# Kernel tuning notes

Hardware: AMD Instinct MI355X
Metric: run time of the kernel (lower is better)

## Reference

```python
import jax, jax.numpy as jnp
import numpy as np

H, C = 4, 32            # heads, per-head out channels
N, E = 25000, 400000    # nodes, edges
NODE_DIM, EDGE_DIM = 256, 64
HC = H * C
IN_DIMS = [NODE_DIM, NODE_DIM + HC, NODE_DIM + HC]


def _conv(h, src, dst, ea, Wq, bq, Wk, bk, Wv, bv, We, Ws, bs):
    """One PyG-style TransformerConv (concat=True, root_weight=True, beta=False)."""
    n = h.shape[0]
    q = (h @ Wq + bq).reshape(n, H, C)
    k = (h @ Wk + bk).reshape(n, H, C)
    v = (h @ Wv + bv).reshape(n, H, C)
    e = (ea @ We).reshape(-1, H, C)            # lin_edge has no bias in PyG
    kj = k[src] + e                             # (E,H,C) key + edge feature
    alpha = jnp.einsum('ehc,ehc->eh', q[dst], kj) / jnp.asarray(np.sqrt(C), h.dtype)
    # segment softmax over incoming edges of each destination node
    amax = jax.ops.segment_max(alpha, dst, num_segments=n)
    ex = jnp.exp(alpha - amax[dst])
    denom = jax.ops.segment_sum(ex, dst, num_segments=n)
    a = ex / (denom[dst] + 1e-16)
    msg = (v[src] + e) * a[:, :, None]          # (E,H,C)
    out = jax.ops.segment_sum(msg, dst, num_segments=n).reshape(n, HC)
    return out + h @ Ws + bs                    # root/skip connection


def setup_inputs() -> dict:
    key = jax.random.key(0)
    ks = iter(jax.random.split(key, 64))
    inp = {}
    inp['x'] = jax.random.normal(next(ks), (N, NODE_DIM), dtype=jnp.float32)
    inp['edge_index'] = jax.random.randint(next(ks), (2, E), 0, N, dtype=jnp.int64)
    inp['edge_attr'] = jax.random.normal(next(ks), (E, EDGE_DIM), dtype=jnp.float32)
    s = 0.05
    for i, din in enumerate(IN_DIMS):
        inp[f'Wq{i}'] = jax.random.normal(next(ks), (din, HC), dtype=jnp.float32) * s
        inp[f'bq{i}'] = jnp.zeros((HC,), jnp.float32)
        inp[f'Wk{i}'] = jax.random.normal(next(ks), (din, HC), dtype=jnp.float32) * s
        inp[f'bk{i}'] = jnp.zeros((HC,), jnp.float32)
        inp[f'Wv{i}'] = jax.random.normal(next(ks), (din, HC), dtype=jnp.float32) * s
        inp[f'bv{i}'] = jnp.zeros((HC,), jnp.float32)
        inp[f'We{i}'] = jax.random.normal(next(ks), (EDGE_DIM, HC), dtype=jnp.float32) * s
        inp[f'Ws{i}'] = jax.random.normal(next(ks), (din, HC), dtype=jnp.float32) * s
        inp[f'bs{i}'] = jnp.zeros((HC,), jnp.float32)
    inp['Wout'] = jax.random.normal(next(ks), (HC, C), dtype=jnp.float32) * s
    inp['bout'] = jnp.zeros((C,), jnp.float32)
    return inp


def reference(x, edge_index, edge_attr,
              Wq0, bq0, Wk0, bk0, Wv0, bv0, We0, Ws0, bs0,
              Wq1, bq1, Wk1, bk1, Wv1, bv1, We1, Ws1, bs1,
              Wq2, bq2, Wk2, bk2, Wv2, bv2, We2, Ws2, bs2,
              Wout, bout):
    src, dst = edge_index[0], edge_index[1]
    params = [
        (Wq0, bq0, Wk0, bk0, Wv0, bv0, We0, Ws0, bs0),
        (Wq1, bq1, Wk1, bk1, Wv1, bv1, We1, Ws1, bs1),
        (Wq2, bq2, Wk2, bk2, Wv2, bv2, We2, Ws2, bs2),
    ]
    h = _conv(x, src, dst, edge_attr, *params[0])
    for p in params[1:]:
        h = _conv(jnp.concatenate([h, x], axis=-1), src, dst, edge_attr, *p)
    return h @ Wout + bout  # (N, output_dim)
```

## Files before the change

kernel.cpp:

```cpp
#include <hip/hip_runtime.h>
#include <hip/hip_bf16.h>
#include <math.h>

#define HCX 128
#define EDX 64
#define KPAD 384

typedef short bf16x8 __attribute__((ext_vector_type(8)));
typedef float f32x4  __attribute__((ext_vector_type(4)));

__device__ __forceinline__ short f2bf(float v) {
    __hip_bfloat16 b = __float2bfloat16(v);
    return *reinterpret_cast<short*>(&b);
}
__device__ __forceinline__ float bf2f(short s) {
    __hip_bfloat16 b = *reinterpret_cast<__hip_bfloat16*>(&s);
    return __bfloat162float(b);
}
__device__ __forceinline__ void gload16(const short* g, short* l) {
    __builtin_amdgcn_global_load_lds((const __attribute__((address_space(1))) void*)g,
                                     (__attribute__((address_space(3))) void*)l, 16, 0, 0);
}
__device__ __forceinline__ float dot4(float4 a, float4 b) {
    return a.x * b.x + a.y * b.y + a.z * b.z + a.w * b.w;
}

__global__ __launch_bounds__(256) void k_zero_deg(int* __restrict__ deg, int n) {
    int t = blockIdx.x * 256 + threadIdx.x;
    if (t < n) deg[t] = 0;
}

__global__ __launch_bounds__(256) void k_hist(const int* __restrict__ dst, int* __restrict__ deg, int nE) {
    int t = blockIdx.x * 256 + threadIdx.x;
    if (t < nE) atomicAdd(&deg[dst[t]], 1);
}

__global__ __launch_bounds__(1024) void k_scan(const int* __restrict__ deg, int* __restrict__ csr_off,
                                               int* __restrict__ cursor, int nN) {
    __shared__ int sums[1024];
    int t = threadIdx.x;
    int chunk = (nN + 1023) >> 10;
    int lo = min(t * chunk, nN), hi = min(lo + chunk, nN);
    int s = 0;
    for (int i = lo; i < hi; ++i) s += deg[i];
    sums[t] = s;
    __syncthreads();
    for (int off = 1; off < 1024; off <<= 1) {
        int v = (t >= off) ? sums[t - off] : 0;
        __syncthreads();
        sums[t] += v;
        __syncthreads();
    }
    int run = (t == 0) ? 0 : sums[t - 1];
    for (int i = lo; i < hi; ++i) {
        csr_off[i] = run; cursor[i] = run;
        run += deg[i];
    }
    if (t == 1023) csr_off[nN] = sums[1023];
}

__global__ __launch_bounds__(256) void k_scatter(const int* __restrict__ dst, const int* __restrict__ src,
                                                 int* __restrict__ cursor,
                                                 int* __restrict__ edge_sorted, int* __restrict__ src_sorted,
                                                 int* __restrict__ dst_sorted, int nE) {
    int t = blockIdx.x * 256 + threadIdx.x;
    if (t < nE) {
        int d = dst[t];
        int pos = atomicAdd(&cursor[d], 1);
        edge_sorted[pos] = t;
        src_sorted[pos]  = src[t];
        dst_sorted[pos]  = d;
    }
}

__global__ __launch_bounds__(256) void k_gather_ea(const float* __restrict__ ea,
                                                   const int* __restrict__ edge_sorted,
                                                   float* __restrict__ ea_s, int nE)
{
    int t = blockIdx.x * 256 + threadIdx.x;
    int i = t >> 4, c = (t & 15) * 4;
    if (i < nE) {
        int eid = edge_sorted[i];
        *(float4*)(ea_s + (size_t)i * EDX + c) = *(const float4*)(ea + (size_t)eid * EDX + c);
    }
}

__global__ __launch_bounds__(256) void k_cvt_h(const float* __restrict__ pH, int has_h,
                                               short* __restrict__ Ah, short* __restrict__ Al,
                                               int nN, int Mpad)
{
    int t = blockIdx.x * 256 + threadIdx.x;
    int row = t >> 5;
    if (row >= Mpad) return;
    int c0 = (t & 31) * 4;
    float4 v = make_float4(0.f, 0.f, 0.f, 0.f);
    if (has_h && row < nN) v = *(const float4*)(pH + (size_t)row * HCX + c0);
    short4 hs, ls;
    hs.x = f2bf(v.x); ls.x = f2bf(v.x - bf2f(hs.x));
    hs.y = f2bf(v.y); ls.y = f2bf(v.y - bf2f(hs.y));
    hs.z = f2bf(v.z); ls.z = f2bf(v.z - bf2f(hs.z));
    hs.w = f2bf(v.w); ls.w = f2bf(v.w - bf2f(hs.w));
    *(short4*)(Ah + (size_t)row * KPAD + c0) = hs;
    *(short4*)(Al + (size_t)row * KPAD + c0) = ls;
}

__global__ __launch_bounds__(256) void k_cvt_x(const float* __restrict__ x,
                                               short* __restrict__ Ah, short* __restrict__ Al,
                                               int nN, int Mpad)
{
    int t = blockIdx.x * 256 + threadIdx.x;
    int row = t >> 6;
    if (row >= Mpad) return;
    int c0 = (t & 63) * 4;
    float4 v = make_float4(0.f, 0.f, 0.f, 0.f);
    if (row < nN) v = *(const float4*)(x + (size_t)row * 256 + c0);
    short4 hs, ls;
    hs.x = f2bf(v.x); ls.x = f2bf(v.x - bf2f(hs.x));
    hs.y = f2bf(v.y); ls.y = f2bf(v.y - bf2f(hs.y));
    hs.z = f2bf(v.z); ls.z = f2bf(v.z - bf2f(hs.z));
    hs.w = f2bf(v.w); ls.w = f2bf(v.w - bf2f(hs.w));
    *(short4*)(Ah + (size_t)row * KPAD + 128 + c0) = hs;
    *(short4*)(Al + (size_t)row * KPAD + 128 + c0) = ls;
}

__global__ __launch_bounds__(384) void k_cvt_W(const float* __restrict__ Wq, const float* __restrict__ Wk,
                                               const float* __restrict__ Wv, const float* __restrict__ Ws,
                                               int koff, int dinW,
                                               short* __restrict__ Wth, short* __restrict__ Wtl)
{
    int col = blockIdx.x;
    int g = col >> 7, c = col & 127;
    const float* W = (g == 0) ? Wq : (g == 1) ? Wk : (g == 2) ? Wv : Ws;
    for (int k = threadIdx.x; k < KPAD; k += blockDim.x) {
        int kr = k - koff;
        float v = (kr >= 0 && kr < dinW) ? W[(size_t)kr * HCX + c] : 0.f;
        short h = f2bf(v);
        Wth[(size_t)col * KPAD + k] = h;
        Wtl[(size_t)col * KPAD + k] = f2bf(v - bf2f(h));
    }
}

__global__ __launch_bounds__(256) void k_gemm(
    const short* __restrict__ Ah, const short* __restrict__ Al,
    const short* __restrict__ Wth, const short* __restrict__ Wtl,
    const float* __restrict__ bq, const float* __restrict__ bk,
    const float* __restrict__ bv, const float* __restrict__ bs,
    float* __restrict__ qkvs, int nN)
{
    __shared__ short AsH[128 * 32];
    __shared__ short AsL[128 * 32];
    __shared__ short BsH[128 * 32];
    __shared__ short BsL[128 * 32];

    const int rowB = blockIdx.x * 128;
    const int g = blockIdx.y;
    const int colB = g * 128;
    const int tid = threadIdx.x;
    const int w = tid >> 6, l = tid & 63;

    f32x4 acc[4][4];
    #pragma unroll
    for (int i = 0; i < 4; ++i)
        #pragma unroll
        for (int j = 0; j < 4; ++j)
            acc[i][j] = (f32x4){0.f, 0.f, 0.f, 0.f};

    const int lrow4 = l >> 2;
    const int gch = (l & 3) ^ ((l >> 3) & 3);
    const int lr = l & 15, kg = l >> 4;

    for (int ks = 0; ks < KPAD / 32; ++ks) {
        const int k0 = ks * 32;
        #pragma unroll
        for (int jj = 0; jj < 2; ++jj) {
            int j = w + jj * 4;
            int rr = j * 16 + lrow4;
            size_t aoff = (size_t)(rowB + rr) * KPAD + k0 + gch * 8;
            size_t boff = (size_t)(colB + rr) * KPAD + k0 + gch * 8;
            gload16(Ah  + aoff, AsH + j * 512);
            gload16(Al  + aoff, AsL + j * 512);
            gload16(Wth + boff, BsH + j * 512);
            gload16(Wtl + boff, BsL + j * 512);
        }
        __syncthreads();

        bf16x8 ah[4], am[4], bh[4], bm[4];
        #pragma unroll
        for (int mi = 0; mi < 4; ++mi) {
            int r = (w >> 1) * 64 + mi * 16 + lr;
            int ch = kg ^ ((r >> 1) & 3);
            int off = r * 32 + ch * 8;
            ah[mi] = *(const bf16x8*)(AsH + off);
            am[mi] = *(const bf16x8*)(AsL + off);
        }
        #pragma unroll
        for (int ni = 0; ni < 4; ++ni) {
            int c = (w & 1) * 64 + ni * 16 + lr;
            int ch = kg ^ ((c >> 1) & 3);
            int off = c * 32 + ch * 8;
            bh[ni] = *(const bf16x8*)(BsH + off);
            bm[ni] = *(const bf16x8*)(BsL + off);
        }
        #pragma unroll
        for (int mi = 0; mi < 4; ++mi)
            #pragma unroll
            for (int ni = 0; ni < 4; ++ni) {
                acc[mi][ni] = __builtin_amdgcn_mfma_f32_16x16x32_bf16(ah[mi], bh[ni], acc[mi][ni], 0, 0, 0);
                acc[mi][ni] = __builtin_amdgcn_mfma_f32_16x16x32_bf16(ah[mi], bm[ni], acc[mi][ni], 0, 0, 0);
                acc[mi][ni] = __builtin_amdgcn_mfma_f32_16x16x32_bf16(am[mi], bh[ni], acc[mi][ni], 0, 0, 0);
            }
        __syncthreads();
    }

    const float* bias = (g == 0) ? bq : (g == 1) ? bk : (g == 2) ? bv : bs;
    float* outp = qkvs + (size_t)g * nN * HCX;
    const int lq = l >> 4;
    #pragma unroll
    for (int mi = 0; mi < 4; ++mi)
        #pragma unroll
        for (int ni = 0; ni < 4; ++ni) {
            int c = (w & 1) * 64 + ni * 16 + lr;
            float bb = bias[c];
            #pragma unroll
            for (int j = 0; j < 4; ++j) {
                int r = rowB + (w >> 1) * 64 + mi * 16 + lq * 4 + j;
                if (r < nN) outp[(size_t)r * HCX + c] = acc[mi][ni][j] + bb;
            }
        }
}

__global__ __launch_bounds__(256) void k_qwe(const float* __restrict__ qpl,
                                             const float* __restrict__ We,
                                             float* __restrict__ qWe, int nN)
{
    __shared__ float Wes[64 * 128];
    __shared__ float qs[16][128];
    for (int i = threadIdx.x; i < 64 * 128; i += 256) {
        int d = i >> 7, c = i & 127;
        Wes[d * 128 + ((c + d) & 127)] = We[i];
    }
    int nb = blockIdx.x * 16;
    for (int i = threadIdx.x; i < 16 * 128; i += 256) {
        int r = i >> 7, c = i & 127;
        int row = nb + r;
        qs[r][c] = (row < nN) ? qpl[(size_t)row * HCX + c] : 0.f;
    }
    __syncthreads();
    int h = threadIdx.x >> 6, d = threadIdx.x & 63;
    const int base = h * 32;
    for (int r = 0; r < 16; ++r) {
        int row = nb + r;
        if (row >= nN) break;
        float s = 0.f;
        #pragma unroll
        for (int c = 0; c < 32; ++c)
            s += qs[r][base + c] * Wes[d * 128 + ((base + c + d) & 127)];
        qWe[(size_t)row * 256 + threadIdx.x] = s;
    }
}

__global__ __launch_bounds__(256) void k_alpha2(
    const float* __restrict__ qkvs, const float* __restrict__ qWe,
    const float* __restrict__ eaS,
    const int* __restrict__ eidx,
    const int* __restrict__ src_sorted, const int* __restrict__ dst_sorted,
    float* __restrict__ expA, int nN, int nE)
{
    int i = blockIdx.x * 256 + threadIdx.x;
    if (i >= nE) return;
    int sn = src_sorted[i], dn = dst_sorted[i];
    int erow = eidx ? eidx[i] : i;

    const float* q = qkvs + (size_t)dn * HCX;
    const float* k = qkvs + (size_t)nN * HCX + (size_t)sn * HCX;
    float r[4];
    #pragma unroll
    for (int h = 0; h < 4; ++h) {
        float4 s4 = make_float4(0.f, 0.f, 0.f, 0.f);
        #pragma unroll
        for (int c = 0; c < 32; c += 4) {
            float4 qv = *(const float4*)(q + h * 32 + c);
            float4 kv = *(const float4*)(k + h * 32 + c);
            s4.x += qv.x * kv.x; s4.y += qv.y * kv.y;
            s4.z += qv.z * kv.z; s4.w += qv.w * kv.w;
        }
        r[h] = s4.x + s4.y + s4.z + s4.w;
    }

    const float* qw = qWe + (size_t)dn * 256;
    const float* ev = eaS + (size_t)erow * EDX;
    float th0 = 0.f, th1 = 0.f, th2 = 0.f, th3 = 0.f;
    #pragma unroll
    for (int d0 = 0; d0 < 64; d0 += 16) {
        float4 a0 = *(const float4*)(ev + d0);
        float4 a1 = *(const float4*)(ev + d0 + 4);
        float4 a2 = *(const float4*)(ev + d0 + 8);
        float4 a3 = *(const float4*)(ev + d0 + 12);
        th0 += dot4(a0, *(const float4*)(qw +   0 + d0)) + dot4(a1, *(const float4*)(qw +   0 + d0 + 4))
             + dot4(a2, *(const float4*)(qw +   0 + d0 + 8)) + dot4(a3, *(const float4*)(qw +   0 + d0 + 12));
        th1 += dot4(a0, *(const float4*)(qw +  64 + d0)) + dot4(a1, *(const float4*)(qw +  64 + d0 + 4))
             + dot4(a2, *(const float4*)(qw +  64 + d0 + 8)) + dot4(a3, *(const float4*)(qw +  64 + d0 + 12));
        th2 += dot4(a0, *(const float4*)(qw + 128 + d0)) + dot4(a1, *(const float4*)(qw + 128 + d0 + 4))
             + dot4(a2, *(const float4*)(qw + 128 + d0 + 8)) + dot4(a3, *(const float4*)(qw + 128 + d0 + 12));
        th3 += dot4(a0, *(const float4*)(qw + 192 + d0)) + dot4(a1, *(const float4*)(qw + 192 + d0 + 4))
             + dot4(a2, *(const float4*)(qw + 192 + d0 + 8)) + dot4(a3, *(const float4*)(qw + 192 + d0 + 12));
    }

    const float scale = 0.17677669529663687f;
    float4 out;
    out.x = __expf((r[0] + th0) * scale);
    out.y = __expf((r[1] + th1) * scale);
    out.z = __expf((r[2] + th2) * scale);
    out.w = __expf((r[3] + th3) * scale);
    *(float4*)(expA + (size_t)i * 4) = out;
}

__global__ __launch_bounds__(256) void k_edge2(
    const float* __restrict__ qkvs, const float* __restrict__ expA,
    const float* __restrict__ eaS, const int* __restrict__ eidx,
    const float* __restrict__ We,
    const int* __restrict__ csr_off, const int* __restrict__ src_sorted,
    float* __restrict__ hout, int nN)
{
    __shared__ float wea_s[4][4][64];
    const int wv = threadIdx.x >> 6, l = threadIdx.x & 63;
    const int n = blockIdx.x * 4 + wv;
    const bool active = n < nN;
    int o0 = 0, o1 = 0;
    if (active) { o0 = csr_off[n]; o1 = csr_off[n + 1]; }

    const float* vpl = qkvs + 2 * (size_t)nN * HCX;
    const int hsel = l >> 5;

    float den0 = 0.f, den1 = 0.f, den2 = 0.f, den3 = 0.f;
    float w0 = 0.f, w1 = 0.f, w2 = 0.f, w3 = 0.f;
    float macc0 = 0.f, macc1 = 0.f;

    #pragma unroll 2
    for (int i = o0; i < o1; ++i) {
        float4 e4 = *(const float4*)(expA + (size_t)i * 4);
        int erow = eidx ? eidx[i] : i;
        int sn  = src_sorted[i];
        float eav = eaS[(size_t)erow * EDX + l];
        float vv0 = vpl[(size_t)sn * HCX + l];
        float vv1 = vpl[(size_t)sn * HCX + 64 + l];

        den0 += e4.x; den1 += e4.y; den2 += e4.z; den3 += e4.w;
        w0 += e4.x * eav; w1 += e4.y * eav; w2 += e4.z * eav; w3 += e4.w * eav;
        float eA = hsel ? e4.y : e4.x;
        float eB = hsel ? e4.w : e4.z;
        macc0 += eA * vv0;
        macc1 += eB * vv1;
    }

    wea_s[wv][0][l] = w0; wea_s[wv][1][l] = w1;
    wea_s[wv][2][l] = w2; wea_s[wv][3][l] = w3;
    __syncthreads();

    float acc1 = macc0, acc2 = macc1;
    const int h1 = hsel, h2 = 2 + hsel;
    #pragma unroll 8
    for (int d = 0; d < 64; ++d) {
        acc1 += wea_s[wv][h1][d] * We[d * HCX + l];
        acc2 += wea_s[wv][h2][d] * We[d * HCX + 64 + l];
    }
    if (active) {
        float d1 = (hsel ? den1 : den0) + 1e-16f;
        float d2 = (hsel ? den3 : den2) + 1e-16f;
        const float* spl = qkvs + 3 * (size_t)nN * HCX + (size_t)n * HCX;
        hout[(size_t)n * HCX + l]      = acc1 / d1 + spl[l];
        hout[(size_t)n * HCX + 64 + l] = acc2 / d2 + spl[64 + l];
    }
}

__global__ __launch_bounds__(256) void k_out(const float* __restrict__ h,
                                             const float* __restrict__ Wout,
                                             const float* __restrict__ bout,
                                             float* __restrict__ out, int nN)
{
    __shared__ float hs[8][128];
    int nb = blockIdx.x * 8;
    for (int i = threadIdx.x; i < 8 * 128; i += 256) {
        int r = i >> 7, c = i & 127;
        int row = nb + r;
        hs[r][c] = (row < nN) ? h[(size_t)row * 128 + c] : 0.f;
    }
    __syncthreads();
    int r = threadIdx.x >> 5, col = threadIdx.x & 31;
    int row = nb + r;
    if (row < nN) {
        float s = bout[col];
        #pragma unroll 16
        for (int c = 0; c < 128; ++c) s += hs[r][c] * Wout[c * 32 + col];
        out[(size_t)row * 32 + col] = s;
    }
}

static inline size_t align_up(size_t v, size_t a) { return (v + a - 1) & ~(a - 1); }

extern "C" void kernel_launch(void* const* d_in, const int* in_sizes, int n_in,
                              void* d_out, int out_size, void* d_ws, size_t ws_size,
                              hipStream_t stream)
{
    const float* x  = (const float*)d_in[0];
    const int*   ei = (const int*)d_in[1];
    const float* ea = (const float*)d_in[2];
    const int nN = in_sizes[0] / 256;
    const int nE = in_sizes[1] / 2;
    const int Mpad = (nN + 127) & ~127;
    const int* src = ei;
    const int* dst = ei + nE;

    char* p = (char*)d_ws;
    size_t off = 0;
    auto take = [&](size_t bytes) { void* r = p + off; off = align_up(off + bytes, 256); return r; };
    int* csr_off     = (int*)take((size_t)(nN + 1) * 4);
    int* cursor      = (int*)take((size_t)nN * 4);
    int* deg         = (int*)take((size_t)nN * 4);
    int* edge_sorted = (int*)take((size_t)nE * 4);
    int* src_sorted  = (int*)take((size_t)nE * 4);
    int* dst_sorted  = (int*)take((size_t)nE * 4);
    float* qkvs = (float*)take((size_t)4 * nN * HCX * 4);
    float* qWe  = (float*)take((size_t)nN * 256 * 4);
    float* expA = (float*)take((size_t)nE * 4 * 4);
    float* h0   = (float*)take((size_t)nN * HCX * 4);
    float* h1   = (float*)take((size_t)nN * HCX * 4);
    short* Ah   = (short*)take((size_t)Mpad * KPAD * 2);
    short* Al   = (short*)take((size_t)Mpad * KPAD * 2);
    short* Wth  = (short*)take((size_t)512 * KPAD * 2);
    short* Wtl  = (short*)take((size_t)512 * KPAD * 2);
    float* ea_s = (float*)take((size_t)nE * EDX * 4);
    const bool use_sorted = (off <= ws_size);
    (void)n_in; (void)out_size;

    k_zero_deg<<<(nN + 255) / 256, 256, 0, stream>>>(deg, nN);
    k_hist<<<(nE + 255) / 256, 256, 0, stream>>>(dst, deg, nE);
    k_scan<<<1, 1024, 0, stream>>>(deg, csr_off, cursor, nN);
    k_scatter<<<(nE + 255) / 256, 256, 0, stream>>>(dst, src, cursor,
                                                    edge_sorted, src_sorted, dst_sorted, nE);

    const float* eaS = use_sorted ? ea_s : ea;
    const int* eidx  = use_sorted ? nullptr : edge_sorted;
    if (use_sorted)
        k_gather_ea<<<(nE * 16 + 255) / 256, 256, 0, stream>>>(ea, edge_sorted, ea_s, nE);

    k_cvt_x<<<(Mpad * 64 + 255) / 256, 256, 0, stream>>>(x, Ah, Al, nN, Mpad);

    auto layer = [&](const float* pH, int has_h, int base, float* hout) {
        const float* Wq = (const float*)d_in[base + 0];
        const float* bq = (const float*)d_in[base + 1];
        const float* Wk = (const float*)d_in[base + 2];
        const float* bk = (const float*)d_in[base + 3];
        const float* Wv = (const float*)d_in[base + 4];
        const float* bv = (const float*)d_in[base + 5];
        const float* We = (const float*)d_in[base + 6];
        const float* Ws = (const float*)d_in[base + 7];
        const float* bs = (const float*)d_in[base + 8];
        int koff = has_h ? 0 : 128;
        int dinW = has_h ? 384 : 256;
        k_cvt_h<<<(Mpad * 32 + 255) / 256, 256, 0, stream>>>(pH, has_h, Ah, Al, nN, Mpad);
        k_cvt_W<<<512, 384, 0, stream>>>(Wq, Wk, Wv, Ws, koff, dinW, Wth, Wtl);
        dim3 gg(Mpad / 128, 4);
        k_gemm<<<gg, 256, 0, stream>>>(Ah, Al, Wth, Wtl, bq, bk, bv, bs, qkvs, nN);
        k_qwe<<<(nN + 15) / 16, 256, 0, stream>>>(qkvs, We, qWe, nN);
        k_alpha2<<<(nE + 255) / 256, 256, 0, stream>>>(qkvs, qWe, eaS, eidx,
                                                       src_sorted, dst_sorted, expA, nN, nE);
        k_edge2<<<(nN + 3) / 4, 256, 0, stream>>>(qkvs, expA, eaS, eidx, We,
                                                  csr_off, src_sorted, hout, nN);
    };

    layer(nullptr, 0, 3,  h0);
    layer(h0, 1,   12, h1);
    layer(h1, 1,   21, h0);

    k_out<<<(nN + 7) / 8, 256, 0, stream>>>(h0, (const float*)d_in[30], (const float*)d_in[31],
                                            (float*)d_out, nN);
}
```

Before: 1.167 ms.

## Store sorted edge attributes as bf16 and split alpha kernel per head pair

The gathered, dst-sorted edge attribute copy is now stored as bf16 instead of fp32, halving the memory traffic of edge-attribute reads in both the alpha and aggregation kernels. The alpha kernel now uses two threads per edge, each handling two heads, which raises parallelism and cuts per-thread register pressure. bf16-to-float conversion is replaced with a plain shift. Precision of the edge attributes drops to bf16, which risks accuracy drift across three layers.

```diff
diff --git a/kernel.cpp b/kernel.cpp
--- a/kernel.cpp
+++ b/kernel.cpp
@@ -14,8 +14,8 @@
     return *reinterpret_cast<short*>(&b);
 }
 __device__ __forceinline__ float bf2f(short s) {
-    __hip_bfloat16 b = *reinterpret_cast<__hip_bfloat16*>(&s);
-    return __bfloat162float(b);
+    unsigned int u = ((unsigned int)(unsigned short)s) << 16;
+    return __uint_as_float(u);
 }
 __device__ __forceinline__ void gload16(const short* g, short* l) {
     __builtin_amdgcn_global_load_lds((const __attribute__((address_space(1))) void*)g,
@@ -73,15 +73,18 @@
     }
 }
 
-__global__ __launch_bounds__(256) void k_gather_ea(const float* __restrict__ ea,
-                                                   const int* __restrict__ edge_sorted,
-                                                   float* __restrict__ ea_s, int nE)
+__global__ __launch_bounds__(256) void k_gather_ea16(const float* __restrict__ ea,
+                                                     const int* __restrict__ edge_sorted,
+                                                     short* __restrict__ ea16, int nE)
 {
     int t = blockIdx.x * 256 + threadIdx.x;
     int i = t >> 4, c = (t & 15) * 4;
     if (i < nE) {
         int eid = edge_sorted[i];
-        *(float4*)(ea_s + (size_t)i * EDX + c) = *(const float4*)(ea + (size_t)eid * EDX + c);
+        float4 v = *(const float4*)(ea + (size_t)eid * EDX + c);
+        short4 s;
+        s.x = f2bf(v.x); s.y = f2bf(v.y); s.z = f2bf(v.z); s.w = f2bf(v.w);
+        *(short4*)(ea16 + (size_t)i * EDX + c) = s;
     }
 }
 
@@ -259,65 +262,67 @@
     }
 }
 
-__global__ __launch_bounds__(256) void k_alpha2(
+__global__ __launch_bounds__(256) void k_alpha3(
     const float* __restrict__ qkvs, const float* __restrict__ qWe,
-    const float* __restrict__ eaS,
+    const short* __restrict__ ea16,
+    const float* __restrict__ eaF,
     const int* __restrict__ eidx,
     const int* __restrict__ src_sorted, const int* __restrict__ dst_sorted,
     float* __restrict__ expA, int nN, int nE)
 {
-    int i = blockIdx.x * 256 + threadIdx.x;
+    int t = blockIdx.x * 256 + threadIdx.x;
+    int i = t >> 1, hp = t & 1;
     if (i >= nE) return;
     int sn = src_sorted[i], dn = dst_sorted[i];
-    int erow = eidx ? eidx[i] : i;
-
-    const float* q = qkvs + (size_t)dn * HCX;
-    const float* k = qkvs + (size_t)nN * HCX + (size_t)sn * HCX;
-    float r[4];
+
+    const float* q = qkvs + (size_t)dn * HCX + hp * 64;
+    const float* k = qkvs + (size_t)nN * HCX + (size_t)sn * HCX + hp * 64;
+    float r0 = 0.f, r1 = 0.f;
     #pragma unroll
-    for (int h = 0; h < 4; ++h) {
-        float4 s4 = make_float4(0.f, 0.f, 0.f, 0.f);
-        #pragma unroll
-        for (int c = 0; c < 32; c += 4) {
-            float4 qv = *(const float4*)(q + h * 32 + c);
-            float4 kv = *(const float4*)(k + h * 32 + c);
-            s4.x += qv.x * kv.x; s4.y += qv.y * kv.y;
-            s4.z += qv.z * kv.z; s4.w += qv.w * kv.w;
-        }
-        r[h] = s4.x + s4.y + s4.z + s4.w;
-    }
-
-    const float* qw = qWe + (size_t)dn * 256;
-    const float* ev = eaS + (size_t)erow * EDX;
-    float th0 = 0.f, th1 = 0.f, th2 = 0.f, th3 = 0.f;
-    #pragma unroll
-    for (int d0 = 0; d0 < 64; d0 += 16) {
-        float4 a0 = *(const float4*)(ev + d0);
-        float4 a1 = *(const float4*)(ev + d0 + 4);
-        float4 a2 = *(const float4*)(ev + d0 + 8);
-        float4 a3 = *(const float4*)(ev + d0 + 12);
-        th0 += dot4(a0, *(const float4*)(qw +   0 + d0)) + dot4(a1, *(const float4*)(qw +   0 + d0 + 4))
-             + dot4(a2, *(const float4*)(qw +   0 + d0 + 8)) + dot4(a3, *(const float4*)(qw +   0 + d0 + 12));
-        th1 += dot4(a0, *(const float4*)(qw +  64 + d0)) + dot4(a1, *(const float4*)(qw +  64 + d0 + 4))
-             + dot4(a2, *(const float4*)(qw +  64 + d0 + 8)) + dot4(a3, *(const float4*)(qw +  64 + d0 + 12));
-        th2 += dot4(a0, *(const float4*)(qw + 128 + d0)) + dot4(a1, *(const float4*)(qw + 128 + d0 + 4))
-             + dot4(a2, *(const float4*)(qw + 128 + d0 + 8)) + dot4(a3, *(const float4*)(qw + 128 + d0 + 12));
-        th3 += dot4(a0, *(const float4*)(qw + 192 + d0)) + dot4(a1, *(const float4*)(qw + 192 + d0 + 4))
-             + dot4(a2, *(const float4*)(qw + 192 + d0 + 8)) + dot4(a3, *(const float4*)(qw + 192 + d0 + 12));
+    for (int c = 0; c < 32; c += 4) {
+        r0 += dot4(*(const float4*)(q + c),      *(const float4*)(k + c));
+        r1 += dot4(*(const float4*)(q + 32 + c), *(const float4*)(k + 32 + c));
+    }
+
+    const float* qw = qWe + (size_t)dn * 256 + hp * 128;
+    float t0 = 0.f, t1 = 0.f;
+    if (ea16) {
+        const short* ev = ea16 + (size_t)i * EDX;
+        #pragma unroll
+        for (int d0 = 0; d0 < 64; d0 += 8) {
+            bf16x8 a8 = *(const bf16x8*)(ev + d0);
+            float4 qa = *(const float4*)(qw + d0);
+            float4 qb = *(const float4*)(qw + d0 + 4);
+            float4 qc = *(const float4*)(qw + 64 + d0);
+            float4 qd = *(const float4*)(qw + 64 + d0 + 4);
+            float a0 = bf2f(a8[0]), a1 = bf2f(a8[1]), a2 = bf2f(a8[2]), a3 = bf2f(a8[3]);
+            float a4 = bf2f(a8[4]), a5 = bf2f(a8[5]), a6 = bf2f(a8[6]), a7 = bf2f(a8[7]);
+            t0 += a0 * qa.x + a1 * qa.y + a2 * qa.z + a3 * qa.w
+                + a4 * qb.x + a5 * qb.y + a6 * qb.z + a7 * qb.w;
+            t1 += a0 * qc.x + a1 * qc.y + a2 * qc.z + a3 * qc.w
+                + a4 * qd.x + a5 * qd.y + a6 * qd.z + a7 * qd.w;
+        }
+    } else {
+        const float* ev = eaF + (size_t)eidx[i] * EDX;
+        #pragma unroll
+        for (int d0 = 0; d0 < 64; d0 += 4) {
+            float4 av = *(const float4*)(ev + d0);
+            t0 += dot4(av, *(const float4*)(qw + d0));
+            t1 += dot4(av, *(const float4*)(qw + 64 + d0));
+        }
     }
 
     const float scale = 0.17677669529663687f;
-    float4 out;
-    out.x = __expf((r[0] + th0) * scale);
-    out.y = __expf((r[1] + th1) * scale);
-    out.z = __expf((r[2] + th2) * scale);
-    out.w = __expf((r[3] + th3) * scale);
-    *(float4*)(expA + (size_t)i * 4) = out;
+    float2 o;
+    o.x = __expf((r0 + t0) * scale);
+    o.y = __expf((r1 + t1) * scale);
+    *(float2*)(expA + (size_t)i * 4 + hp * 2) = o;
 }
 
 __global__ __launch_bounds__(256) void k_edge2(
     const float* __restrict__ qkvs, const float* __restrict__ expA,
-    const float* __restrict__ eaS, const int* __restrict__ eidx,
+    const short* __restrict__ ea16, const float* __restrict__ eaF,
+    const int* __restrict__ eidx,
     const float* __restrict__ We,
     const int* __restrict__ csr_off, const int* __restrict__ src_sorted,
     float* __restrict__ hout, int nN)
@@ -336,22 +341,29 @@
     float w0 = 0.f, w1 = 0.f, w2 = 0.f, w3 = 0.f;
     float macc0 = 0.f, macc1 = 0.f;
 
-    #pragma unroll 2
-    for (int i = o0; i < o1; ++i) {
-        float4 e4 = *(const float4*)(expA + (size_t)i * 4);
-        int erow = eidx ? eidx[i] : i;
-        int sn  = src_sorted[i];
-        float eav = eaS[(size_t)erow * EDX + l];
-        float vv0 = vpl[(size_t)sn * HCX + l];
-        float vv1 = vpl[(size_t)sn * HCX + 64 + l];
-
-        den0 += e4.x; den1 += e4.y; den2 += e4.z; den3 += e4.w;
-        w0 += e4.x * eav; w1 += e4.y * eav; w2 += e4.z * eav; w3 += e4.w * eav;
-        float eA = hsel ? e4.y : e4.x;
-        float eB = hsel ? e4.w : e4.z;
-        macc0 += eA * vv0;
-        macc1 += eB * vv1;
-    }
+#define EDGE_BODY(EAV_EXPR)                                          \
+    _Pragma("unroll 2")                                              \
+    for (int i = o0; i < o1; ++i) {                                  \
+        float4 e4 = *(const float4*)(expA + (size_t)i * 4);          \
+        int sn = src_sorted[i];                                      \
+        float eav = (EAV_EXPR);                                      \
+        float vv0 = vpl[(size_t)sn * HCX + l];                       \
+        float vv1 = vpl[(size_t)sn * HCX + 64 + l];                  \
+        den0 += e4.x; den1 += e4.y; den2 += e4.z; den3 += e4.w;      \
+        w0 += e4.x * eav; w1 += e4.y * eav;                          \
+        w2 += e4.z * eav; w3 += e4.w * eav;                          \
+        float eA = hsel ? e4.y : e4.x;                               \
+        float eB = hsel ? e4.w : e4.z;                               \
+        macc0 += eA * vv0;                                           \
+        macc1 += eB * vv1;                                           \
+    }
+
+    if (ea16) {
+        EDGE_BODY(bf2f(ea16[(size_t)i * EDX + l]))
+    } else {
+        EDGE_BODY(eaF[(size_t)eidx[i] * EDX + l])
+    }
+#undef EDGE_BODY
 
     wea_s[wv][0][l] = w0; wea_s[wv][1][l] = w1;
     wea_s[wv][2][l] = w2; wea_s[wv][3][l] = w3;
@@ -429,7 +441,7 @@
     short* Al   = (short*)take((size_t)Mpad * KPAD * 2);
     short* Wth  = (short*)take((size_t)512 * KPAD * 2);
     short* Wtl  = (short*)take((size_t)512 * KPAD * 2);
-    float* ea_s = (float*)take((size_t)nE * EDX * 4);
+    short* ea16 = (short*)take((size_t)nE * EDX * 2);
     const bool use_sorted = (off <= ws_size);
     (void)n_in; (void)out_size;
 
@@ -439,10 +451,10 @@
     k_scatter<<<(nE + 255) / 256, 256, 0, stream>>>(dst, src, cursor,
                                                     edge_sorted, src_sorted, dst_sorted, nE);
 
-    const float* eaS = use_sorted ? ea_s : ea;
-    const int* eidx  = use_sorted ? nullptr : edge_sorted;
+    short* ea16p    = use_sorted ? ea16 : nullptr;
+    const int* eidx = use_sorted ? nullptr : edge_sorted;
     if (use_sorted)
-        k_gather_ea<<<(nE * 16 + 255) / 256, 256, 0, stream>>>(ea, edge_sorted, ea_s, nE);
+        k_gather_ea16<<<(nE * 16 + 255) / 256, 256, 0, stream>>>(ea, edge_sorted, ea16, nE);
 
     k_cvt_x<<<(Mpad * 64 + 255) / 256, 256, 0, stream>>>(x, Ah, Al, nN, Mpad);
 
@@ -463,9 +475,9 @@
         dim3 gg(Mpad / 128, 4);
         k_gemm<<<gg, 256, 0, stream>>>(Ah, Al, Wth, Wtl, bq, bk, bv, bs, qkvs, nN);
         k_qwe<<<(nN + 15) / 16, 256, 0, stream>>>(qkvs, We, qWe, nN);
-        k_alpha2<<<(nE + 255) / 256, 256, 0, stream>>>(qkvs, qWe, eaS, eidx,
-                                                       src_sorted, dst_sorted, expA, nN, nE);
-        k_edge2<<<(nN + 3) / 4, 256, 0, stream>>>(qkvs, expA, eaS, eidx, We,
+        k_alpha3<<<(nE * 2 + 255) / 256, 256, 0, stream>>>(qkvs, qWe, ea16p, ea, eidx,
+                                                           src_sorted, dst_sorted, expA, nN, nE);
+        k_edge2<<<(nN + 3) / 4, 256, 0, stream>>>(qkvs, expA, ea16p, ea, eidx, We,
                                                   csr_off, src_sorted, hout, nN);
     };
 
```

New measurement: 1.107 ms. -5.1%, faster.
